# Performance work log

Measured on AMD Instinct MI355X. Metric: run time of the kernel, lower is better.

Reference implementation:

```python
import jax, jax.numpy as jnp
import numpy as np

D_MODEL = 1024
N_HEADS = 16
D_HEAD = D_MODEL // N_HEADS
MODES = 32


def setup_inputs() -> dict:
    key = jax.random.key(0)
    ks = jax.random.split(key, 7)
    B, L = 4, 4096
    s = 1.0 / np.sqrt(D_MODEL)
    return {
        "q_in": jax.random.normal(ks[0], (B, L, D_MODEL), dtype=jnp.float32),
        "Wv": jax.random.uniform(ks[1], (D_MODEL, D_MODEL), jnp.float32, -s, s),
        "bv": jax.random.uniform(ks[2], (D_MODEL,), jnp.float32, -s, s),
        "Wo": jax.random.uniform(ks[3], (D_MODEL, D_MODEL), jnp.float32, -s, s),
        "bo": jax.random.uniform(ks[4], (D_MODEL,), jnp.float32, -s, s),
        "w_real": jax.random.normal(ks[5], (N_HEADS, MODES, D_HEAD), dtype=jnp.float32) * 0.02,
        "w_imag": jax.random.normal(ks[6], (N_HEADS, MODES, D_HEAD), dtype=jnp.float32) * 0.02,
    }


def reference(q_in, Wv, bv, Wo, bo, w_real, w_imag):
    B, L, dm = q_in.shape
    # v projection -> [B, H, L, Dh]
    v = (q_in @ Wv.T + bv).reshape(B, L, N_HEADS, D_HEAD).transpose(0, 2, 1, 3)
    # rFFT over time axis; keep only lowest MODES frequencies
    v_ft = jnp.fft.rfft(v, axis=2)                      # [B, H, L//2+1, Dh] complex
    w = (w_real + 1j * w_imag)[None]                    # [1, H, MODES, Dh]
    out_ft = v_ft[:, :, :MODES, :] * w                  # truncated spectrum
    # irfft zero-pads the truncated spectrum up to n//2+1 (== torch's zeros_like + slice-assign)
    out = jnp.fft.irfft(out_ft, n=L, axis=2)            # [B, H, L, Dh]
    out = out.transpose(0, 2, 1, 3).reshape(B, L, dm)
    return out @ Wo.T + bo
```

## Files before the change

### kernel.cpp

```cpp
#include <hip/hip_runtime.h>
#include <math.h>


typedef __attribute__((ext_vector_type(8))) short bf16x8;
typedef __attribute__((ext_vector_type(8))) unsigned short ushort8;
typedef __attribute__((ext_vector_type(4))) float f32x4;

__device__ __forceinline__ unsigned short f2bf(float x) {
    union { float f; unsigned int u; } c; c.f = x;
    unsigned int u = c.u + 0x7FFFu + ((c.u >> 16) & 1u);
    return (unsigned short)(u >> 16);
}

__global__ __launch_bounds__(256) void k_init(unsigned short* __restrict__ F,
                                              unsigned short* __restrict__ G,
                                              float* __restrict__ A,
                                              float* __restrict__ C,
                                              float* __restrict__ Z) {
    int idx = blockIdx.x * 256 + threadIdx.x;
    const float w0 = 1.5339807878856412e-3f;
    {
        int j = idx >> 12, t = idx & 4095, k = j >> 1;
        int r = (k * t) & 4095;
        float s, c; sincosf((float)r * w0, &s, &c);
        F[idx] = f2bf((j & 1) ? -s : c);
    }
    {
        int j = idx & 63, k = j >> 1;
        int t = idx >> 6;
        int r = (k * t) & 4095;
        float s, c; sincosf((float)r * w0, &s, &c);
        float ck = (k == 0) ? (1.0f / 4096.0f) : (2.0f / 4096.0f);
        float v = (j & 1) ? ((k == 0) ? 0.0f : -ck * s) : ck * c;
        G[idx] = f2bf(v);
    }
    A[idx] = 0.0f;
    C[idx] = 0.0f;
    Z[idx] = 0.0f;
}

__global__ __launch_bounds__(256) void k_dft_fwd(const float* __restrict__ q,
                                                 const unsigned short* __restrict__ F,
                                                 float* __restrict__ A) {
    int blk = blockIdx.x;
    int kp = blk & 15, nt = (blk >> 4) & 7, b = blk >> 7;
    int tid = threadIdx.x, lane = tid & 63, w = tid >> 6;
    int lm = lane & 15, q4 = lane >> 4;
    int n0 = nt * 128 + w * 32;
    int t0 = kp * 256;
    f32x4 acc[4][2] = {};
    #pragma unroll 2
    for (int ks = 0; ks < 8; ++ks) {
        int tb = t0 + ks * 32 + q4 * 8;
        bf16x8 af[4];
        #pragma unroll
        for (int mt = 0; mt < 4; ++mt)
            af[mt] = *(const bf16x8*)&F[(mt * 16 + lm) * 4096 + tb];
        bf16x8 bq[2];
        #pragma unroll
        for (int ntt = 0; ntt < 2; ++ntt) {
            const float* qp = &q[(size_t)(b * 4096 + tb) * 1024 + n0 + ntt * 16 + lm];
            float f0 = qp[0 * 1024], f1 = qp[1 * 1024], f2 = qp[2 * 1024], f3 = qp[3 * 1024];
            float f4 = qp[4 * 1024], f5 = qp[5 * 1024], f6 = qp[6 * 1024], f7 = qp[7 * 1024];
            union { unsigned int u[4]; bf16x8 v; } cv;
            cv.u[0] = (unsigned)f2bf(f0) | ((unsigned)f2bf(f1) << 16);
            cv.u[1] = (unsigned)f2bf(f2) | ((unsigned)f2bf(f3) << 16);
            cv.u[2] = (unsigned)f2bf(f4) | ((unsigned)f2bf(f5) << 16);
            cv.u[3] = (unsigned)f2bf(f6) | ((unsigned)f2bf(f7) << 16);
            bq[ntt] = cv.v;
        }
        #pragma unroll
        for (int mt = 0; mt < 4; ++mt)
            #pragma unroll
            for (int ntt = 0; ntt < 2; ++ntt)
                acc[mt][ntt] = __builtin_amdgcn_mfma_f32_16x16x32_bf16(
                    af[mt], bq[ntt], acc[mt][ntt], 0, 0, 0);
    }
    #pragma unroll
    for (int mt = 0; mt < 4; ++mt)
        #pragma unroll
        for (int ntt = 0; ntt < 2; ++ntt)
            #pragma unroll
            for (int r = 0; r < 4; ++r) {
                int j = mt * 16 + q4 * 4 + r;
                int n = n0 + ntt * 16 + lm;
                atomicAdd(&A[(b * 64 + j) * 1024 + n], acc[mt][ntt][r]);
            }
}

template<int ABF16>
__global__ __launch_bounds__(256) void k_gemm_bt(const void* __restrict__ Ain,
                                                 const float* __restrict__ Bmat,
                                                 float* __restrict__ Cout) {
    __shared__ __align__(16) unsigned short At[64 * 40];
    __shared__ __align__(16) unsigned short Wt[128 * 40];
    int blk = blockIdx.x;
    int kp = blk & 7, nt = (blk >> 3) & 7, mt = blk >> 6;
    int m0 = mt * 64, n0 = nt * 128, k0 = kp * 128;
    int tid = threadIdx.x, lane = tid & 63, w = tid >> 6;
    int lm = lane & 15, q4 = lane >> 4;
    int ma = tid >> 2, ka = (tid & 3) * 8;
    int nw = tid >> 1, kw = (tid & 1) * 16;
    f32x4 acc[4][2] = {};
    for (int ks = 0; ks < 4; ++ks) {
        int kb = k0 + ks * 32;
        if (ABF16) {
            ushort8 v = *(const ushort8*)&((const unsigned short*)Ain)[(m0 + ma) * 1024 + kb + ka];
            *(ushort8*)&At[ma * 40 + ka] = v;
        } else {
            const float* Af = (const float*)Ain;
            float4 x0 = *(const float4*)&Af[(m0 + ma) * 1024 + kb + ka];
            float4 x1 = *(const float4*)&Af[(m0 + ma) * 1024 + kb + ka + 4];
            ushort8 v;
            v[0]=f2bf(x0.x); v[1]=f2bf(x0.y); v[2]=f2bf(x0.z); v[3]=f2bf(x0.w);
            v[4]=f2bf(x1.x); v[5]=f2bf(x1.y); v[6]=f2bf(x1.z); v[7]=f2bf(x1.w);
            *(ushort8*)&At[ma * 40 + ka] = v;
        }
        {
            const float4* wp = (const float4*)&Bmat[(n0 + nw) * 1024 + kb + kw];
            float4 x0 = wp[0], x1 = wp[1], x2 = wp[2], x3 = wp[3];
            ushort8 v0, v1;
            v0[0]=f2bf(x0.x); v0[1]=f2bf(x0.y); v0[2]=f2bf(x0.z); v0[3]=f2bf(x0.w);
            v0[4]=f2bf(x1.x); v0[5]=f2bf(x1.y); v0[6]=f2bf(x1.z); v0[7]=f2bf(x1.w);
            v1[0]=f2bf(x2.x); v1[1]=f2bf(x2.y); v1[2]=f2bf(x2.z); v1[3]=f2bf(x2.w);
            v1[4]=f2bf(x3.x); v1[5]=f2bf(x3.y); v1[6]=f2bf(x3.z); v1[7]=f2bf(x3.w);
            *(ushort8*)&Wt[nw * 40 + kw]     = v0;
            *(ushort8*)&Wt[nw * 40 + kw + 8] = v1;
        }
        __syncthreads();
        bf16x8 af[4], bf[2];
        #pragma unroll
        for (int mti = 0; mti < 4; ++mti)
            af[mti] = *(const bf16x8*)&At[(mti * 16 + lm) * 40 + q4 * 8];
        #pragma unroll
        for (int ntt = 0; ntt < 2; ++ntt)
            bf[ntt] = *(const bf16x8*)&Wt[(w * 32 + ntt * 16 + lm) * 40 + q4 * 8];
        #pragma unroll
        for (int mti = 0; mti < 4; ++mti)
            #pragma unroll
            for (int ntt = 0; ntt < 2; ++ntt)
                acc[mti][ntt] = __builtin_amdgcn_mfma_f32_16x16x32_bf16(
                    af[mti], bf[ntt], acc[mti][ntt], 0, 0, 0);
        __syncthreads();
    }
    #pragma unroll
    for (int mti = 0; mti < 4; ++mti)
        #pragma unroll
        for (int ntt = 0; ntt < 2; ++ntt)
            #pragma unroll
            for (int r = 0; r < 4; ++r) {
                int m = m0 + mti * 16 + q4 * 4 + r;
                int n = n0 + w * 32 + ntt * 16 + lm;
                atomicAdd(&Cout[m * 1024 + n], acc[mti][ntt][r]);
            }
}

__global__ __launch_bounds__(256) void k_cmul(const float* __restrict__ C,
                                              const float* __restrict__ bv,
                                              const float* __restrict__ wr,
                                              const float* __restrict__ wi,
                                              unsigned short* __restrict__ Y) {
    int idx = blockIdx.x * 256 + threadIdx.x;
    int n = idx & 1023, k = (idx >> 10) & 31, b = idx >> 15;
    int rowr = (b * 64 + 2 * k) * 1024 + n;
    int rowi = rowr + 1024;
    float re = C[rowr];
    float im = C[rowi];
    if (k == 0) re += 4096.0f * bv[n];
    int h = n >> 6, dh = n & 63;
    float a = wr[(h * 32 + k) * 64 + dh];
    float c = wi[(h * 32 + k) * 64 + dh];
    Y[rowr] = f2bf(re * a - im * c);
    Y[rowi] = f2bf(re * c + im * a);
}

__global__ __launch_bounds__(256) void k_dft_inv(const unsigned short* __restrict__ G,
                                                 const float* __restrict__ Zf,
                                                 const float* __restrict__ bo,
                                                 float* __restrict__ out) {
    __shared__ __align__(16) unsigned short Gt[128 * 72];
    __shared__ __align__(16) unsigned short ZT[128 * 72];
    int blk = blockIdx.x;
    int nt = blk & 7, tt = (blk >> 3) & 31, b = blk >> 8;
    int n0 = nt * 128, t0 = tt * 128;
    int tid = threadIdx.x, lane = tid & 63, w = tid >> 6;
    int lm = lane & 15, q4 = lane >> 4;
    {
        int ttl = tid >> 1, jj = (tid & 1) * 32;
        #pragma unroll
        for (int i = 0; i < 4; ++i) {
            ushort8 v = *(const ushort8*)&G[(t0 + ttl) * 64 + jj + i * 8];
            *(ushort8*)&Gt[ttl * 72 + jj + i * 8] = v;
        }
    }
    {
        int jp = tid & 31, hi = tid >> 5;
        int j = jp * 2, nn0 = hi * 16;
        const float* r0 = &Zf[(b * 64 + j) * 1024 + n0 + nn0];
        const float* r1 = r0 + 1024;
        float za[16], zb[16];
        #pragma unroll
        for (int i = 0; i < 4; ++i) {
            float4 va = ((const float4*)r0)[i];
            float4 vb = ((const float4*)r1)[i];
            za[4*i+0] = va.x; za[4*i+1] = va.y; za[4*i+2] = va.z; za[4*i+3] = va.w;
            zb[4*i+0] = vb.x; zb[4*i+1] = vb.y; zb[4*i+2] = vb.z; zb[4*i+3] = vb.w;
        }
        #pragma unroll
        for (int i = 0; i < 16; ++i) {
            unsigned int v = (unsigned)f2bf(za[i]) | ((unsigned)f2bf(zb[i]) << 16);
            *(unsigned int*)&ZT[(nn0 + i) * 72 + j] = v;
        }
    }
    __syncthreads();
    int wt0 = (w >> 1) * 64, wn0 = (w & 1) * 64;
    f32x4 acc[4][4] = {};
    #pragma unroll
    for (int ks = 0; ks < 2; ++ks) {
        bf16x8 af[4], bf[4];
        #pragma unroll
        for (int mt = 0; mt < 4; ++mt)
            af[mt] = *(const bf16x8*)&Gt[(wt0 + mt * 16 + lm) * 72 + ks * 32 + q4 * 8];
        #pragma unroll
        for (int ntt = 0; ntt < 4; ++ntt)
            bf[ntt] = *(const bf16x8*)&ZT[(wn0 + ntt * 16 + lm) * 72 + ks * 32 + q4 * 8];
        #pragma unroll
        for (int mt = 0; mt < 4; ++mt)
            #pragma unroll
            for (int ntt = 0; ntt < 4; ++ntt)
                acc[mt][ntt] = __builtin_amdgcn_mfma_f32_16x16x32_bf16(
                    af[mt], bf[ntt], acc[mt][ntt], 0, 0, 0);
    }
    #pragma unroll
    for (int ntt = 0; ntt < 4; ++ntt) {
        int n = n0 + wn0 + ntt * 16 + lm;
        float bov = bo[n];
        #pragma unroll
        for (int mt = 0; mt < 4; ++mt)
            #pragma unroll
            for (int r = 0; r < 4; ++r) {
                int t = t0 + wt0 + mt * 16 + q4 * 4 + r;
                out[(size_t)(b * 4096 + t) * 1024 + n] = acc[mt][ntt][r] + bov;
            }
    }
}

extern "C" void kernel_launch(void* const* d_in, const int* in_sizes, int n_in,
                              void* d_out, int out_size, void* d_ws, size_t ws_size,
                              hipStream_t stream) {
    const float* q  = (const float*)d_in[0];
    const float* Wv = (const float*)d_in[1];
    const float* bv = (const float*)d_in[2];
    const float* Wo = (const float*)d_in[3];
    const float* bo = (const float*)d_in[4];
    const float* wr = (const float*)d_in[5];
    const float* wi = (const float*)d_in[6];
    float* out = (float*)d_out;

    char* ws = (char*)d_ws;
    unsigned short* F  = (unsigned short*)(ws);
    unsigned short* G  = (unsigned short*)(ws + (512 << 10));
    float*          A  = (float*)(ws + (1u << 20));
    float*          C  = (float*)(ws + (2u << 20));
    float*          Z  = (float*)(ws + (3u << 20));
    unsigned short* Y  = (unsigned short*)(ws + (4u << 20));

    hipLaunchKernelGGL(k_init,         dim3(1024), dim3(256), 0, stream, F, G, A, C, Z);
    hipLaunchKernelGGL(k_dft_fwd,      dim3(512),  dim3(256), 0, stream, q, F, A);
    hipLaunchKernelGGL((k_gemm_bt<0>), dim3(256),  dim3(256), 0, stream, (const void*)A, Wv, C);
    hipLaunchKernelGGL(k_cmul,         dim3(512),  dim3(256), 0, stream, C, bv, wr, wi, Y);
    hipLaunchKernelGGL((k_gemm_bt<1>), dim3(256),  dim3(256), 0, stream, (const void*)Y, Wo, Z);
    hipLaunchKernelGGL(k_dft_inv,      dim3(1024), dim3(256), 0, stream, G, Z, bo, out);
}
```

Before: 175.4 us.

## Replace atomic split-K with partial buffers, fuse cmul into second GEMM

The two small GEMMs now write split-K partials to separate buffers instead of using atomicAdd into zeroed outputs. The complex mode multiply and bias are folded into the second GEMM's A-tile load, which removes the k_cmul launch and the Y intermediate. The inverse DFT sums the four Z partials on load, and k_init no longer zeroes C and Z and uses fast __sinf/__cosf. The forward DFT halves the n-tile per block and doubles the grid for more parallelism, at the cost of re-reading the F fragments more often. The GEMMs drop to 128 blocks with longer K loops, which lowers occupancy, and the fast trig gives slightly less accurate twiddles.

```diff
diff --git a/kernel.cpp b/kernel.cpp
--- a/kernel.cpp
+++ b/kernel.cpp
@@ -14,41 +14,37 @@
 
 __global__ __launch_bounds__(256) void k_init(unsigned short* __restrict__ F,
                                               unsigned short* __restrict__ G,
-                                              float* __restrict__ A,
-                                              float* __restrict__ C,
-                                              float* __restrict__ Z) {
+                                              float* __restrict__ A) {
     int idx = blockIdx.x * 256 + threadIdx.x;
     const float w0 = 1.5339807878856412e-3f;
     {
         int j = idx >> 12, t = idx & 4095, k = j >> 1;
         int r = (k * t) & 4095;
-        float s, c; sincosf((float)r * w0, &s, &c);
-        F[idx] = f2bf((j & 1) ? -s : c);
+        float ang = (float)r * w0;
+        F[idx] = f2bf((j & 1) ? -__sinf(ang) : __cosf(ang));
     }
     {
         int j = idx & 63, k = j >> 1;
         int t = idx >> 6;
         int r = (k * t) & 4095;
-        float s, c; sincosf((float)r * w0, &s, &c);
+        float ang = (float)r * w0;
         float ck = (k == 0) ? (1.0f / 4096.0f) : (2.0f / 4096.0f);
-        float v = (j & 1) ? ((k == 0) ? 0.0f : -ck * s) : ck * c;
+        float v = (j & 1) ? ((k == 0) ? 0.0f : -ck * __sinf(ang)) : ck * __cosf(ang);
         G[idx] = f2bf(v);
     }
     A[idx] = 0.0f;
-    C[idx] = 0.0f;
-    Z[idx] = 0.0f;
 }
 
 __global__ __launch_bounds__(256) void k_dft_fwd(const float* __restrict__ q,
                                                  const unsigned short* __restrict__ F,
                                                  float* __restrict__ A) {
     int blk = blockIdx.x;
-    int kp = blk & 15, nt = (blk >> 4) & 7, b = blk >> 7;
+    int kp = blk & 15, nt = (blk >> 4) & 15, b = blk >> 8;
     int tid = threadIdx.x, lane = tid & 63, w = tid >> 6;
     int lm = lane & 15, q4 = lane >> 4;
-    int n0 = nt * 128 + w * 32;
+    int n0 = nt * 64 + w * 16;
     int t0 = kp * 256;
-    f32x4 acc[4][2] = {};
+    f32x4 acc[4] = {};
     #pragma unroll 2
     for (int ks = 0; ks < 8; ++ks) {
         int tb = t0 + ks * 32 + q4 * 8;
@@ -56,68 +52,54 @@
         #pragma unroll
         for (int mt = 0; mt < 4; ++mt)
             af[mt] = *(const bf16x8*)&F[(mt * 16 + lm) * 4096 + tb];
-        bf16x8 bq[2];
-        #pragma unroll
-        for (int ntt = 0; ntt < 2; ++ntt) {
-            const float* qp = &q[(size_t)(b * 4096 + tb) * 1024 + n0 + ntt * 16 + lm];
-            float f0 = qp[0 * 1024], f1 = qp[1 * 1024], f2 = qp[2 * 1024], f3 = qp[3 * 1024];
-            float f4 = qp[4 * 1024], f5 = qp[5 * 1024], f6 = qp[6 * 1024], f7 = qp[7 * 1024];
-            union { unsigned int u[4]; bf16x8 v; } cv;
-            cv.u[0] = (unsigned)f2bf(f0) | ((unsigned)f2bf(f1) << 16);
-            cv.u[1] = (unsigned)f2bf(f2) | ((unsigned)f2bf(f3) << 16);
-            cv.u[2] = (unsigned)f2bf(f4) | ((unsigned)f2bf(f5) << 16);
-            cv.u[3] = (unsigned)f2bf(f6) | ((unsigned)f2bf(f7) << 16);
-            bq[ntt] = cv.v;
-        }
-        #pragma unroll
-        for (int mt = 0; mt < 4; ++mt)
-            #pragma unroll
-            for (int ntt = 0; ntt < 2; ++ntt)
-                acc[mt][ntt] = __builtin_amdgcn_mfma_f32_16x16x32_bf16(
-                    af[mt], bq[ntt], acc[mt][ntt], 0, 0, 0);
+        const float* qp = &q[(size_t)(b * 4096 + tb) * 1024 + n0 + lm];
+        float f0 = qp[0 * 1024], f1 = qp[1 * 1024], f2 = qp[2 * 1024], f3 = qp[3 * 1024];
+        float f4 = qp[4 * 1024], f5 = qp[5 * 1024], f6 = qp[6 * 1024], f7 = qp[7 * 1024];
+        union { unsigned int u[4]; bf16x8 v; } cv;
+        cv.u[0] = (unsigned)f2bf(f0) | ((unsigned)f2bf(f1) << 16);
+        cv.u[1] = (unsigned)f2bf(f2) | ((unsigned)f2bf(f3) << 16);
+        cv.u[2] = (unsigned)f2bf(f4) | ((unsigned)f2bf(f5) << 16);
+        cv.u[3] = (unsigned)f2bf(f6) | ((unsigned)f2bf(f7) << 16);
+        bf16x8 bq = cv.v;
+        #pragma unroll
+        for (int mt = 0; mt < 4; ++mt)
+            acc[mt] = __builtin_amdgcn_mfma_f32_16x16x32_bf16(af[mt], bq, acc[mt], 0, 0, 0);
     }
     #pragma unroll
     for (int mt = 0; mt < 4; ++mt)
         #pragma unroll
-        for (int ntt = 0; ntt < 2; ++ntt)
-            #pragma unroll
-            for (int r = 0; r < 4; ++r) {
-                int j = mt * 16 + q4 * 4 + r;
-                int n = n0 + ntt * 16 + lm;
-                atomicAdd(&A[(b * 64 + j) * 1024 + n], acc[mt][ntt][r]);
-            }
-}
-
-template<int ABF16>
-__global__ __launch_bounds__(256) void k_gemm_bt(const void* __restrict__ Ain,
-                                                 const float* __restrict__ Bmat,
-                                                 float* __restrict__ Cout) {
+        for (int r = 0; r < 4; ++r) {
+            int j = mt * 16 + q4 * 4 + r;
+            int n = n0 + lm;
+            atomicAdd(&A[(b * 64 + j) * 1024 + n], acc[mt][r]);
+        }
+}
+
+__global__ __launch_bounds__(256) void k_gemm0(const float* __restrict__ A,
+                                               const float* __restrict__ Wv,
+                                               float* __restrict__ P_C) {
     __shared__ __align__(16) unsigned short At[64 * 40];
     __shared__ __align__(16) unsigned short Wt[128 * 40];
     int blk = blockIdx.x;
-    int kp = blk & 7, nt = (blk >> 3) & 7, mt = blk >> 6;
-    int m0 = mt * 64, n0 = nt * 128, k0 = kp * 128;
+    int kp = blk & 3, nt = (blk >> 2) & 7, mt = blk >> 5;
+    int m0 = mt * 64, n0 = nt * 128, k0 = kp * 256;
     int tid = threadIdx.x, lane = tid & 63, w = tid >> 6;
     int lm = lane & 15, q4 = lane >> 4;
     int ma = tid >> 2, ka = (tid & 3) * 8;
     int nw = tid >> 1, kw = (tid & 1) * 16;
     f32x4 acc[4][2] = {};
-    for (int ks = 0; ks < 4; ++ks) {
+    for (int ks = 0; ks < 8; ++ks) {
         int kb = k0 + ks * 32;
-        if (ABF16) {
-            ushort8 v = *(const ushort8*)&((const unsigned short*)Ain)[(m0 + ma) * 1024 + kb + ka];
-            *(ushort8*)&At[ma * 40 + ka] = v;
-        } else {
-            const float* Af = (const float*)Ain;
-            float4 x0 = *(const float4*)&Af[(m0 + ma) * 1024 + kb + ka];
-            float4 x1 = *(const float4*)&Af[(m0 + ma) * 1024 + kb + ka + 4];
+        {
+            float4 x0 = *(const float4*)&A[(m0 + ma) * 1024 + kb + ka];
+            float4 x1 = *(const float4*)&A[(m0 + ma) * 1024 + kb + ka + 4];
             ushort8 v;
             v[0]=f2bf(x0.x); v[1]=f2bf(x0.y); v[2]=f2bf(x0.z); v[3]=f2bf(x0.w);
             v[4]=f2bf(x1.x); v[5]=f2bf(x1.y); v[6]=f2bf(x1.z); v[7]=f2bf(x1.w);
             *(ushort8*)&At[ma * 40 + ka] = v;
         }
         {
-            const float4* wp = (const float4*)&Bmat[(n0 + nw) * 1024 + kb + kw];
+            const float4* wp = (const float4*)&Wv[(n0 + nw) * 1024 + kb + kw];
             float4 x0 = wp[0], x1 = wp[1], x2 = wp[2], x3 = wp[3];
             ushort8 v0, v1;
             v0[0]=f2bf(x0.x); v0[1]=f2bf(x0.y); v0[2]=f2bf(x0.z); v0[3]=f2bf(x0.w);
@@ -151,31 +133,106 @@
             for (int r = 0; r < 4; ++r) {
                 int m = m0 + mti * 16 + q4 * 4 + r;
                 int n = n0 + w * 32 + ntt * 16 + lm;
-                atomicAdd(&Cout[m * 1024 + n], acc[mti][ntt][r]);
-            }
-}
-
-__global__ __launch_bounds__(256) void k_cmul(const float* __restrict__ C,
-                                              const float* __restrict__ bv,
-                                              const float* __restrict__ wr,
-                                              const float* __restrict__ wi,
-                                              unsigned short* __restrict__ Y) {
-    int idx = blockIdx.x * 256 + threadIdx.x;
-    int n = idx & 1023, k = (idx >> 10) & 31, b = idx >> 15;
-    int rowr = (b * 64 + 2 * k) * 1024 + n;
-    int rowi = rowr + 1024;
-    float re = C[rowr];
-    float im = C[rowi];
-    if (k == 0) re += 4096.0f * bv[n];
-    int h = n >> 6, dh = n & 63;
-    float a = wr[(h * 32 + k) * 64 + dh];
-    float c = wi[(h * 32 + k) * 64 + dh];
-    Y[rowr] = f2bf(re * a - im * c);
-    Y[rowi] = f2bf(re * c + im * a);
+                P_C[(size_t)kp * 262144 + m * 1024 + n] = acc[mti][ntt][r];
+            }
+}
+
+__global__ __launch_bounds__(256) void k_gemm1(const float* __restrict__ P_C,
+                                               const float* __restrict__ bv,
+                                               const float* __restrict__ wr,
+                                               const float* __restrict__ wi,
+                                               const float* __restrict__ Wo,
+                                               float* __restrict__ P_Z) {
+    __shared__ __align__(16) unsigned short At[64 * 40];
+    __shared__ __align__(16) unsigned short Wt[128 * 40];
+    int blk = blockIdx.x;
+    int kp = blk & 3, nt = (blk >> 2) & 7, mt = blk >> 5;
+    int m0 = mt * 64, n0 = nt * 128, k0 = kp * 256;
+    int tid = threadIdx.x, lane = tid & 63, w = tid >> 6;
+    int lm = lane & 15, q4 = lane >> 4;
+    int ma = tid >> 2, ka = (tid & 3) * 8;
+    int nw = tid >> 1, kw = (tid & 1) * 16;
+    int odd = ma & 1, kmode = ma >> 1;
+    size_t rbase = (size_t)(m0 + (ma & ~1)) * 1024;
+    f32x4 acc[4][2] = {};
+    for (int ks = 0; ks < 8; ++ks) {
+        int kb = k0 + ks * 32;
+        {
+            int n = kb + ka;
+            float re[8] = {}, im[8] = {};
+            #pragma unroll
+            for (int s = 0; s < 4; ++s) {
+                const float* pr = &P_C[(size_t)s * 262144 + rbase + n];
+                float4 r0 = ((const float4*)pr)[0], r1 = ((const float4*)pr)[1];
+                const float* pi = pr + 1024;
+                float4 i0 = ((const float4*)pi)[0], i1 = ((const float4*)pi)[1];
+                re[0]+=r0.x; re[1]+=r0.y; re[2]+=r0.z; re[3]+=r0.w;
+                re[4]+=r1.x; re[5]+=r1.y; re[6]+=r1.z; re[7]+=r1.w;
+                im[0]+=i0.x; im[1]+=i0.y; im[2]+=i0.z; im[3]+=i0.w;
+                im[4]+=i1.x; im[5]+=i1.y; im[6]+=i1.z; im[7]+=i1.w;
+            }
+            if (kmode == 0) {
+                float4 b0 = ((const float4*)&bv[n])[0], b1 = ((const float4*)&bv[n])[1];
+                re[0]+=4096.f*b0.x; re[1]+=4096.f*b0.y; re[2]+=4096.f*b0.z; re[3]+=4096.f*b0.w;
+                re[4]+=4096.f*b1.x; re[5]+=4096.f*b1.y; re[6]+=4096.f*b1.z; re[7]+=4096.f*b1.w;
+            }
+            int h = n >> 6, dh = n & 63;
+            const float* pa = &wr[(h * 32 + kmode) * 64 + dh];
+            const float* pc = &wi[(h * 32 + kmode) * 64 + dh];
+            float4 a0 = ((const float4*)pa)[0], a1 = ((const float4*)pa)[1];
+            float4 c0 = ((const float4*)pc)[0], c1 = ((const float4*)pc)[1];
+            float av[8] = {a0.x,a0.y,a0.z,a0.w,a1.x,a1.y,a1.z,a1.w};
+            float cv[8] = {c0.x,c0.y,c0.z,c0.w,c1.x,c1.y,c1.z,c1.w};
+            ushort8 v;
+            #pragma unroll
+            for (int i = 0; i < 8; ++i) {
+                float val = odd ? (re[i] * cv[i] + im[i] * av[i])
+                                : (re[i] * av[i] - im[i] * cv[i]);
+                v[i] = f2bf(val);
+            }
+            *(ushort8*)&At[ma * 40 + ka] = v;
+        }
+        {
+            const float4* wp = (const float4*)&Wo[(n0 + nw) * 1024 + kb + kw];
+            float4 x0 = wp[0], x1 = wp[1], x2 = wp[2], x3 = wp[3];
+            ushort8 v0, v1;
+            v0[0]=f2bf(x0.x); v0[1]=f2bf(x0.y); v0[2]=f2bf(x0.z); v0[3]=f2bf(x0.w);
+            v0[4]=f2bf(x1.x); v0[5]=f2bf(x1.y); v0[6]=f2bf(x1.z); v0[7]=f2bf(x1.w);
+            v1[0]=f2bf(x2.x); v1[1]=f2bf(x2.y); v1[2]=f2bf(x2.z); v1[3]=f2bf(x2.w);
+            v1[4]=f2bf(x3.x); v1[5]=f2bf(x3.y); v1[6]=f2bf(x3.z); v1[7]=f2bf(x3.w);
+            *(ushort8*)&Wt[nw * 40 + kw]     = v0;
+            *(ushort8*)&Wt[nw * 40 + kw + 8] = v1;
+        }
+        __syncthreads();
+        bf16x8 af[4], bf[2];
+        #pragma unroll
+        for (int mti = 0; mti < 4; ++mti)
+            af[mti] = *(const bf16x8*)&At[(mti * 16 + lm) * 40 + q4 * 8];
+        #pragma unroll
+        for (int ntt = 0; ntt < 2; ++ntt)
+            bf[ntt] = *(const bf16x8*)&Wt[(w * 32 + ntt * 16 + lm) * 40 + q4 * 8];
+        #pragma unroll
+        for (int mti = 0; mti < 4; ++mti)
+            #pragma unroll
+            for (int ntt = 0; ntt < 2; ++ntt)
+                acc[mti][ntt] = __builtin_amdgcn_mfma_f32_16x16x32_bf16(
+                    af[mti], bf[ntt], acc[mti][ntt], 0, 0, 0);
+        __syncthreads();
+    }
+    #pragma unroll
+    for (int mti = 0; mti < 4; ++mti)
+        #pragma unroll
+        for (int ntt = 0; ntt < 2; ++ntt)
+            #pragma unroll
+            for (int r = 0; r < 4; ++r) {
+                int m = m0 + mti * 16 + q4 * 4 + r;
+                int n = n0 + w * 32 + ntt * 16 + lm;
+                P_Z[(size_t)kp * 262144 + m * 1024 + n] = acc[mti][ntt][r];
+            }
 }
 
 __global__ __launch_bounds__(256) void k_dft_inv(const unsigned short* __restrict__ G,
-                                                 const float* __restrict__ Zf,
+                                                 const float* __restrict__ P_Z,
                                                  const float* __restrict__ bo,
                                                  float* __restrict__ out) {
     __shared__ __align__(16) unsigned short Gt[128 * 72];
@@ -196,15 +253,19 @@
     {
         int jp = tid & 31, hi = tid >> 5;
         int j = jp * 2, nn0 = hi * 16;
-        const float* r0 = &Zf[(b * 64 + j) * 1024 + n0 + nn0];
-        const float* r1 = r0 + 1024;
-        float za[16], zb[16];
-        #pragma unroll
-        for (int i = 0; i < 4; ++i) {
-            float4 va = ((const float4*)r0)[i];
-            float4 vb = ((const float4*)r1)[i];
-            za[4*i+0] = va.x; za[4*i+1] = va.y; za[4*i+2] = va.z; za[4*i+3] = va.w;
-            zb[4*i+0] = vb.x; zb[4*i+1] = vb.y; zb[4*i+2] = vb.z; zb[4*i+3] = vb.w;
+        size_t zoff = (size_t)(b * 64 + j) * 1024 + n0 + nn0;
+        float za[16] = {}, zb[16] = {};
+        #pragma unroll
+        for (int s = 0; s < 4; ++s) {
+            const float* r0 = &P_Z[(size_t)s * 262144 + zoff];
+            const float* r1 = r0 + 1024;
+            #pragma unroll
+            for (int i = 0; i < 4; ++i) {
+                float4 va = ((const float4*)r0)[i];
+                float4 vb = ((const float4*)r1)[i];
+                za[4*i+0] += va.x; za[4*i+1] += va.y; za[4*i+2] += va.z; za[4*i+3] += va.w;
+                zb[4*i+0] += vb.x; zb[4*i+1] += vb.y; zb[4*i+2] += vb.z; zb[4*i+3] += vb.w;
+            }
         }
         #pragma unroll
         for (int i = 0; i < 16; ++i) {
@@ -258,17 +319,15 @@
     float* out = (float*)d_out;
 
     char* ws = (char*)d_ws;
-    unsigned short* F  = (unsigned short*)(ws);
-    unsigned short* G  = (unsigned short*)(ws + (512 << 10));
-    float*          A  = (float*)(ws + (1u << 20));
-    float*          C  = (float*)(ws + (2u << 20));
-    float*          Z  = (float*)(ws + (3u << 20));
-    unsigned short* Y  = (unsigned short*)(ws + (4u << 20));
-
-    hipLaunchKernelGGL(k_init,         dim3(1024), dim3(256), 0, stream, F, G, A, C, Z);
-    hipLaunchKernelGGL(k_dft_fwd,      dim3(512),  dim3(256), 0, stream, q, F, A);
-    hipLaunchKernelGGL((k_gemm_bt<0>), dim3(256),  dim3(256), 0, stream, (const void*)A, Wv, C);
-    hipLaunchKernelGGL(k_cmul,         dim3(512),  dim3(256), 0, stream, C, bv, wr, wi, Y);
-    hipLaunchKernelGGL((k_gemm_bt<1>), dim3(256),  dim3(256), 0, stream, (const void*)Y, Wo, Z);
-    hipLaunchKernelGGL(k_dft_inv,      dim3(1024), dim3(256), 0, stream, G, Z, bo, out);
-}
+    unsigned short* F   = (unsigned short*)(ws);
+    unsigned short* G   = (unsigned short*)(ws + (512 << 10));
+    float*          A   = (float*)(ws + (1u << 20));
+    float*          P_C = (float*)(ws + (2u << 20));
+    float*          P_Z = (float*)(ws + (6u << 20));
+
+    hipLaunchKernelGGL(k_init,    dim3(1024), dim3(256), 0, stream, F, G, A);
+    hipLaunchKernelGGL(k_dft_fwd, dim3(1024), dim3(256), 0, stream, q, F, A);
+    hipLaunchKernelGGL(k_gemm0,   dim3(128),  dim3(256), 0, stream, A, Wv, P_C);
+    hipLaunchKernelGGL(k_gemm1,   dim3(128),  dim3(256), 0, stream, P_C, bv, wr, wi, Wo, P_Z);
+    hipLaunchKernelGGL(k_dft_inv, dim3(1024), dim3(256), 0, stream, G, P_Z, bo, out);
+}
```

Result: slower. 194.0 us (+10.6%).
